# Kernel tuning notes

Hardware: AMD Instinct MI355X
Metric: run time of the kernel (lower is better)

## Reference

```python
import jax, jax.numpy as jnp
import numpy as np

N, D = 8192, 128


def setup_inputs() -> dict:
    key = jax.random.key(0)
    kx, kw, kb = jax.random.split(key, 3)
    x = jax.random.normal(kx, (N, D), dtype=jnp.float32)
    # scale projection weights so attention logits are O(1) (avoids softmax saturation)
    W = jax.random.normal(kw, (3 * D, D), dtype=jnp.float32) * 0.02
    b = jax.random.normal(kb, (3 * D,), dtype=jnp.float32) * 0.02
    return {"x": x, "W": W, "b": b}


def reference(x, W, b):
    # fused QKV projection: nn.Linear(d, 3d) -> x @ W.T + b
    qkv = x @ W.T + b              # [N, 3d]
    q, k, v = jnp.split(qkv, 3, axis=-1)  # each [N, d]
    # the original performs unscaled attention (no 1/sqrt(d)); the tiled
    # online-softmax loop computes exactly softmax(q k^T) @ v.
    s = q @ k.T                    # [N, N]
    p = jax.nn.softmax(s, axis=-1)
    return p @ v                   # [N, d]
```

## Files before the change

### kernel.cpp

```cpp
#include <hip/hip_runtime.h>
#include <hip/hip_bf16.h>

#define NROWS 8192
#define DIM 128

typedef short short8 __attribute__((ext_vector_type(8)));
typedef float f32x4 __attribute__((ext_vector_type(4)));
typedef unsigned short ushort4v __attribute__((ext_vector_type(4)));

__device__ __forceinline__ short8 asbf8(uint4 v) { return __builtin_bit_cast(short8, v); }

__device__ __forceinline__ unsigned cvtpk_bf16(float lo, float hi) {
  unsigned r;
  asm("v_cvt_pk_bf16_f32 %0, %1, %2" : "=v"(r) : "v"(lo), "v"(hi));
  return r;
}
__device__ __forceinline__ void pl32swap(unsigned& a, unsigned& b) {
  asm("v_permlane32_swap_b32 %0, %1" : "+v"(a), "+v"(b));
}
__device__ __forceinline__ void pl16swap(unsigned& a, unsigned& b) {
  asm("v_permlane16_swap_b32 %0, %1" : "+v"(a), "+v"(b));
}
__device__ __forceinline__ void gload_lds16(const void* g, void* l) {
  __builtin_amdgcn_global_load_lds(
      (const __attribute__((address_space(1))) void*)g,
      (__attribute__((address_space(3))) void*)l, 16, 0, 0);
}

__global__ __launch_bounds__(256) void qkv_proj(
    const float* __restrict__ x, const float* __restrict__ W, const float* __restrict__ bias,
    unsigned short* __restrict__ Q, unsigned short* __restrict__ K, unsigned short* __restrict__ Vt)
{
  __shared__ uint4 sX[64 * 16];
  __shared__ uint4 sW[128 * 16];

  const int mt = blockIdx.x;
  const int ct = blockIdx.y;
  const int t = threadIdx.x;

  const float4* xg = (const float4*)(x + (size_t)mt * 64 * DIM);
  const float4* wg = (const float4*)(W + (size_t)ct * 128 * DIM);
#pragma unroll
  for (int j = 0; j < 4; j++) {
    int s = t + 256 * j; int m = s >> 4, c = s & 15;
    float4 a = xg[m * 32 + 2 * c], b = xg[m * 32 + 2 * c + 1];
    sX[m * 16 + (c ^ (m & 7))] =
        (uint4){cvtpk_bf16(a.x, a.y), cvtpk_bf16(a.z, a.w), cvtpk_bf16(b.x, b.y), cvtpk_bf16(b.z, b.w)};
  }
#pragma unroll
  for (int j = 0; j < 8; j++) {
    int s = t + 256 * j; int n = s >> 4, c = s & 15;
    float4 a = wg[n * 32 + 2 * c], b = wg[n * 32 + 2 * c + 1];
    sW[n * 16 + (c ^ (n & 7))] =
        (uint4){cvtpk_bf16(a.x, a.y), cvtpk_bf16(a.z, a.w), cvtpk_bf16(b.x, b.y), cvtpk_bf16(b.z, b.w)};
  }
  __syncthreads();

  const int w = t >> 6, l = t & 63;
  const int r = l & 15, g = l >> 4, rx = r & 7;

  if (ct < 2) {
    uint4 xf[4];
#pragma unroll
    for (int f = 0; f < 4; f++) xf[f] = sX[(w * 16 + r) * 16 + ((f * 4 + g) ^ rx)];
    unsigned short* dst = (ct == 0) ? Q : K;
    const float scale = (ct == 0) ? 1.44269504088896f : 1.0f;
    const int m = mt * 64 + w * 16 + r;
#pragma unroll
    for (int ns = 0; ns < 8; ns++) {
      f32x4 acc = (f32x4){0.f, 0.f, 0.f, 0.f};
#pragma unroll
      for (int f = 0; f < 4; f++) {
        uint4 af = sW[(ns * 16 + r) * 16 + ((f * 4 + g) ^ rx)];
        acc = __builtin_amdgcn_mfma_f32_16x16x32_bf16(asbf8(af), asbf8(xf[f]), acc, 0, 0, 0);
      }
      float4 bv = *(const float4*)&bias[ct * 128 + ns * 16 + 4 * g];
      uint2 pk;
      pk.x = cvtpk_bf16((acc[0] + bv.x) * scale, (acc[1] + bv.y) * scale);
      pk.y = cvtpk_bf16((acc[2] + bv.z) * scale, (acc[3] + bv.w) * scale);
      *(uint2*)&dst[(size_t)m * DIM + ns * 16 + 4 * g] = pk;
    }
  } else {
    uint4 xf[4][4];
#pragma unroll
    for (int ms = 0; ms < 4; ms++)
#pragma unroll
      for (int f = 0; f < 4; f++) xf[ms][f] = sX[(ms * 16 + r) * 16 + ((f * 4 + g) ^ rx)];
#pragma unroll
    for (int u = 0; u < 2; u++) {
      const int n = w * 32 + u * 16 + r;
      uint4 wf[4];
#pragma unroll
      for (int f = 0; f < 4; f++) wf[f] = sW[n * 16 + ((f * 4 + g) ^ rx)];
      const float bv = bias[256 + n];
#pragma unroll
      for (int ms = 0; ms < 4; ms++) {
        f32x4 acc = (f32x4){0.f, 0.f, 0.f, 0.f};
#pragma unroll
        for (int f = 0; f < 4; f++)
          acc = __builtin_amdgcn_mfma_f32_16x16x32_bf16(asbf8(xf[ms][f]), asbf8(wf[f]), acc, 0, 0, 0);
        uint2 pk;
        pk.x = cvtpk_bf16(acc[0] + bv, acc[1] + bv);
        pk.y = cvtpk_bf16(acc[2] + bv, acc[3] + bv);
        *(uint2*)&Vt[(size_t)n * NROWS + mt * 64 + ms * 16 + 4 * g] = pk;
      }
    }
  }
}

__global__ __launch_bounds__(512, 2) void attn(
    const unsigned short* __restrict__ Q, const unsigned short* __restrict__ K,
    const unsigned short* __restrict__ Vt,
    unsigned short* __restrict__ Opb, float* __restrict__ Lp,
    float* __restrict__ outDirect, int kvlen)
{
  __shared__ uint4 sK[64 * 16];
  __shared__ uint4 sV[2][128 * 8];

  const int t = threadIdx.x;
  const int w = t >> 6, l = t & 63;
  const int r = l & 15, g = l >> 4;
  const int qt = blockIdx.x, sp = blockIdx.y;
  const int qbase = qt * 256 + w * 32;
  const int kb0 = sp * kvlen;
  const int rx = r & 7;

  const unsigned short* kgp[2];
  const unsigned short* vgp[2];
#pragma unroll
  for (int j = 0; j < 2; j++) {
    int p = t + 512 * j;
    int krow = p >> 4, kc16 = (p & 15) ^ (krow & 7);
    kgp[j] = K + (size_t)(kb0 + krow) * DIM + kc16 * 8;
    int vrow = p >> 3, vd16 = (p & 7) ^ (vrow & 7);
    vgp[j] = Vt + (size_t)vrow * NROWS + kb0 + vd16 * 8;
  }

  uint4 qf[2][4];
#pragma unroll
  for (int u = 0; u < 2; u++) {
    const uint4* Qv = (const uint4*)(Q + (size_t)(qbase + u * 16 + r) * DIM);
#pragma unroll
    for (int f = 0; f < 4; f++) qf[u][f] = Qv[f * 4 + g];
  }

  float lsum[2] = {0.f, 0.f};
  f32x4 oacc[2][8];
#pragma unroll
  for (int u = 0; u < 2; u++)
#pragma unroll
    for (int dc = 0; dc < 8; dc++) oacc[u][dc] = (f32x4){0.f, 0.f, 0.f, 0.f};

  const int niter = kvlen >> 6;

#pragma unroll
  for (int j = 0; j < 2; j++) {
    gload_lds16(kgp[j], (uint4*)sK + (t + 512 * j));
    gload_lds16(vgp[j], (uint4*)sV[0] + (t + 512 * j));
  }
  __syncthreads();

  int cur = 0;
  for (int it = 0; it < niter; ++it) {
    if (it + 1 < niter) {
      const size_t voff = (size_t)(it + 1) * 64;
#pragma unroll
      for (int j = 0; j < 2; j++)
        gload_lds16(vgp[j] + voff, (uint4*)sV[cur ^ 1] + (t + 512 * j));
    }

    f32x4 sacc[2][4];
#pragma unroll
    for (int u = 0; u < 2; u++)
#pragma unroll
      for (int kc = 0; kc < 4; kc++) sacc[u][kc] = (f32x4){0.f, 0.f, 0.f, 0.f};
#pragma unroll
    for (int kc = 0; kc < 4; kc++)
#pragma unroll
      for (int f = 0; f < 4; f++) {
        uint4 kf = sK[(kc * 16 + r) * 16 + ((f * 4 + g) ^ rx)];
        sacc[0][kc] = __builtin_amdgcn_mfma_f32_16x16x32_bf16(asbf8(kf), asbf8(qf[0][f]), sacc[0][kc], 0, 0, 0);
        sacc[1][kc] = __builtin_amdgcn_mfma_f32_16x16x32_bf16(asbf8(kf), asbf8(qf[1][f]), sacc[1][kc], 0, 0, 0);
      }

    __syncthreads();
    if (it + 1 < niter) {
      const size_t koff = (size_t)(it + 1) * 64 * DIM;
#pragma unroll
      for (int j = 0; j < 2; j++)
        gload_lds16(kgp[j] + koff, (uint4*)sK + (t + 512 * j));
    }

    unsigned c32[2][4][2];
#pragma unroll
    for (int u = 0; u < 2; u++)
#pragma unroll
      for (int kc = 0; kc < 4; kc++) {
        float p0 = __builtin_amdgcn_exp2f(sacc[u][kc][0]);
        float p1 = __builtin_amdgcn_exp2f(sacc[u][kc][1]);
        float p2 = __builtin_amdgcn_exp2f(sacc[u][kc][2]);
        float p3 = __builtin_amdgcn_exp2f(sacc[u][kc][3]);
        lsum[u] += (p0 + p1) + (p2 + p3);
        c32[u][kc][0] = cvtpk_bf16(p0, p1);
        c32[u][kc][1] = cvtpk_bf16(p2, p3);
      }

    uint4 bfrag[2][2];
#pragma unroll
    for (int u = 0; u < 2; u++)
#pragma unroll
      for (int ka = 0; ka < 2; ka++) {
        unsigned x0 = c32[u][2 * ka][0],     x1 = c32[u][2 * ka][1];
        unsigned y0 = c32[u][2 * ka + 1][0], y1 = c32[u][2 * ka + 1][1];
        pl32swap(x0, y0);
        pl16swap(x0, y0);
        pl32swap(x1, y1);
        pl16swap(x1, y1);
        bfrag[u][ka] = (uint4){x0, x1, y0, y1};
      }

#pragma unroll
    for (int dc = 0; dc < 8; dc++) {
      uint4 vf0 = sV[cur][(dc * 16 + r) * 8 + (g ^ rx)];
      uint4 vf1 = sV[cur][(dc * 16 + r) * 8 + ((4 + g) ^ rx)];
      oacc[0][dc] = __builtin_amdgcn_mfma_f32_16x16x32_bf16(asbf8(vf0), asbf8(bfrag[0][0]), oacc[0][dc], 0, 0, 0);
      oacc[0][dc] = __builtin_amdgcn_mfma_f32_16x16x32_bf16(asbf8(vf1), asbf8(bfrag[0][1]), oacc[0][dc], 0, 0, 0);
      oacc[1][dc] = __builtin_amdgcn_mfma_f32_16x16x32_bf16(asbf8(vf0), asbf8(bfrag[1][0]), oacc[1][dc], 0, 0, 0);
      oacc[1][dc] = __builtin_amdgcn_mfma_f32_16x16x32_bf16(asbf8(vf1), asbf8(bfrag[1][1]), oacc[1][dc], 0, 0, 0);
    }

    __syncthreads();
    cur ^= 1;
  }

#pragma unroll
  for (int u = 0; u < 2; u++) {
    float v = lsum[u];
    v += __shfl_xor(v, 16);
    v += __shfl_xor(v, 32);
    lsum[u] = v;
  }

  if (outDirect) {
#pragma unroll
    for (int u = 0; u < 2; u++) {
      float inv = 1.f / lsum[u];
      int q = qbase + u * 16 + r;
#pragma unroll
      for (int dc = 0; dc < 8; dc++) {
        f32x4 o = oacc[u][dc] * inv;
        *(f32x4*)&outDirect[(size_t)q * DIM + dc * 16 + 4 * g] = o;
      }
    }
  } else {
#pragma unroll
    for (int u = 0; u < 2; u++) {
      int q = qbase + u * 16 + r;
      unsigned short* po = Opb + ((size_t)sp * NROWS + q) * DIM;
#pragma unroll
      for (int dc = 0; dc < 8; dc++) {
        uint2 pk;
        pk.x = cvtpk_bf16(oacc[u][dc][0], oacc[u][dc][1]);
        pk.y = cvtpk_bf16(oacc[u][dc][2], oacc[u][dc][3]);
        *(uint2*)&po[dc * 16 + 4 * g] = pk;
      }
      if (g == 0) Lp[(size_t)sp * NROWS + q] = lsum[u];
    }
  }
}

__global__ __launch_bounds__(256) void combine(
    const unsigned short* __restrict__ Opb, const float* __restrict__ Lp,
    float* __restrict__ out, int S)
{
  int gid = blockIdx.x * 256 + threadIdx.x;
  int q = gid >> 5, d4 = gid & 31;
  float den = 0.f, n0 = 0.f, n1 = 0.f, n2 = 0.f, n3 = 0.f;
  for (int s = 0; s < S; s++) {
    den += Lp[(size_t)s * NROWS + q];
    ushort4v h = *(const ushort4v*)&Opb[((size_t)s * NROWS + q) * DIM + d4 * 4];
    n0 += __builtin_bit_cast(float, (unsigned)h[0] << 16);
    n1 += __builtin_bit_cast(float, (unsigned)h[1] << 16);
    n2 += __builtin_bit_cast(float, (unsigned)h[2] << 16);
    n3 += __builtin_bit_cast(float, (unsigned)h[3] << 16);
  }
  float inv = 1.f / den;
  float4 o = {n0 * inv, n1 * inv, n2 * inv, n3 * inv};
  *(float4*)&out[(size_t)q * DIM + d4 * 4] = o;
}

extern "C" void kernel_launch(void* const* d_in, const int* in_sizes, int n_in,
                              void* d_out, int out_size, void* d_ws, size_t ws_size,
                              hipStream_t stream)
{
  (void)in_sizes; (void)n_in; (void)out_size;
  const float* x = (const float*)d_in[0];
  const float* W = (const float*)d_in[1];
  const float* b = (const float*)d_in[2];
  float* out = (float*)d_out;
  char* ws = (char*)d_ws;

  unsigned short* Q  = (unsigned short*)ws;
  unsigned short* K  = Q + (size_t)NROWS * DIM;
  unsigned short* Vt = K + (size_t)NROWS * DIM;
  const size_t qkvB = (size_t)3 * NROWS * DIM * 2;

  auto need = [&](int S) {
    return qkvB + (size_t)S * NROWS * DIM * 2 + (size_t)S * NROWS * 4;
  };
  int S; bool direct = false;
  if      (ws_size >= need(16)) S = 16;
  else if (ws_size >= need(8))  S = 8;
  else if (ws_size >= need(4))  S = 4;
  else if (ws_size >= need(2))  S = 2;
  else if (ws_size >= need(1))  S = 1;
  else { S = 1; direct = true; }

  unsigned short* Opb = (unsigned short*)(ws + qkvB);
  float* Lp = (float*)(Opb + (size_t)S * NROWS * DIM);

  qkv_proj<<<dim3(128, 3), 256, 0, stream>>>(x, W, b, Q, K, Vt);
  attn<<<dim3(32, S), 512, 0, stream>>>(Q, K, Vt, Opb, Lp,
                                        direct ? out : nullptr, NROWS / S);
  if (!direct) combine<<<1024, 256, 0, stream>>>(Opb, Lp, out, S);
}
```

Before: 64.59 us.

## Halve attention block and KV tile, double-buffer K and V, add MFMA priority

Shrinks the attention block from 8 to 4 waves (128 query rows) and the KV tile from 64 to 32 keys, which doubles the grid along the query axis. K is now double-buffered alongside V, so both next tiles are prefetched at the top of each iteration and the mid-iteration barrier is gone. s_setprio wraps the MFMA sections to favour matrix issue. The aim is fewer barriers and more resident blocks; the cost is twice as many iterations and K/V tiles re-read from global memory by twice as many blocks.

```diff
diff --git a/kernel.cpp b/kernel.cpp
--- a/kernel.cpp
+++ b/kernel.cpp
@@ -108,20 +108,20 @@
   }
 }
 
-__global__ __launch_bounds__(512, 2) void attn(
+__global__ __launch_bounds__(256, 4) void attn(
     const unsigned short* __restrict__ Q, const unsigned short* __restrict__ K,
     const unsigned short* __restrict__ Vt,
     unsigned short* __restrict__ Opb, float* __restrict__ Lp,
     float* __restrict__ outDirect, int kvlen)
 {
-  __shared__ uint4 sK[64 * 16];
-  __shared__ uint4 sV[2][128 * 8];
+  __shared__ uint4 sK[2][32 * 16];
+  __shared__ uint4 sV[2][128 * 4];
 
   const int t = threadIdx.x;
   const int w = t >> 6, l = t & 63;
   const int r = l & 15, g = l >> 4;
   const int qt = blockIdx.x, sp = blockIdx.y;
-  const int qbase = qt * 256 + w * 32;
+  const int qbase = qt * 128 + w * 32;
   const int kb0 = sp * kvlen;
   const int rx = r & 7;
 
@@ -129,11 +129,11 @@
   const unsigned short* vgp[2];
 #pragma unroll
   for (int j = 0; j < 2; j++) {
-    int p = t + 512 * j;
+    int p = t + 256 * j;
     int krow = p >> 4, kc16 = (p & 15) ^ (krow & 7);
     kgp[j] = K + (size_t)(kb0 + krow) * DIM + kc16 * 8;
-    int vrow = p >> 3, vd16 = (p & 7) ^ (vrow & 7);
-    vgp[j] = Vt + (size_t)vrow * NROWS + kb0 + vd16 * 8;
+    int vrow = p >> 2, vs = (p & 3) ^ (vrow & 3);
+    vgp[j] = Vt + (size_t)vrow * NROWS + kb0 + vs * 8;
   }
 
   uint4 qf[2][4];
@@ -151,51 +151,49 @@
 #pragma unroll
     for (int dc = 0; dc < 8; dc++) oacc[u][dc] = (f32x4){0.f, 0.f, 0.f, 0.f};
 
-  const int niter = kvlen >> 6;
+  const int niter = kvlen >> 5;
 
 #pragma unroll
   for (int j = 0; j < 2; j++) {
-    gload_lds16(kgp[j], (uint4*)sK + (t + 512 * j));
-    gload_lds16(vgp[j], (uint4*)sV[0] + (t + 512 * j));
+    gload_lds16(kgp[j], (uint4*)sK[0] + (t + 256 * j));
+    gload_lds16(vgp[j], (uint4*)sV[0] + (t + 256 * j));
   }
   __syncthreads();
 
   int cur = 0;
   for (int it = 0; it < niter; ++it) {
     if (it + 1 < niter) {
-      const size_t voff = (size_t)(it + 1) * 64;
-#pragma unroll
-      for (int j = 0; j < 2; j++)
-        gload_lds16(vgp[j] + voff, (uint4*)sV[cur ^ 1] + (t + 512 * j));
-    }
-
-    f32x4 sacc[2][4];
+      const size_t koff = (size_t)(it + 1) * 32 * DIM;
+      const size_t voff = (size_t)(it + 1) * 32;
+      const int nb = cur ^ 1;
+#pragma unroll
+      for (int j = 0; j < 2; j++) {
+        gload_lds16(kgp[j] + koff, (uint4*)sK[nb] + (t + 256 * j));
+        gload_lds16(vgp[j] + voff, (uint4*)sV[nb] + (t + 256 * j));
+      }
+    }
+
+    f32x4 sacc[2][2];
 #pragma unroll
     for (int u = 0; u < 2; u++)
 #pragma unroll
-      for (int kc = 0; kc < 4; kc++) sacc[u][kc] = (f32x4){0.f, 0.f, 0.f, 0.f};
-#pragma unroll
-    for (int kc = 0; kc < 4; kc++)
+      for (int kc = 0; kc < 2; kc++) sacc[u][kc] = (f32x4){0.f, 0.f, 0.f, 0.f};
+    __builtin_amdgcn_s_setprio(1);
+#pragma unroll
+    for (int kc = 0; kc < 2; kc++)
 #pragma unroll
       for (int f = 0; f < 4; f++) {
-        uint4 kf = sK[(kc * 16 + r) * 16 + ((f * 4 + g) ^ rx)];
+        uint4 kf = sK[cur][(kc * 16 + r) * 16 + ((f * 4 + g) ^ rx)];
         sacc[0][kc] = __builtin_amdgcn_mfma_f32_16x16x32_bf16(asbf8(kf), asbf8(qf[0][f]), sacc[0][kc], 0, 0, 0);
         sacc[1][kc] = __builtin_amdgcn_mfma_f32_16x16x32_bf16(asbf8(kf), asbf8(qf[1][f]), sacc[1][kc], 0, 0, 0);
       }
-
-    __syncthreads();
-    if (it + 1 < niter) {
-      const size_t koff = (size_t)(it + 1) * 64 * DIM;
-#pragma unroll
-      for (int j = 0; j < 2; j++)
-        gload_lds16(kgp[j] + koff, (uint4*)sK + (t + 512 * j));
-    }
-
-    unsigned c32[2][4][2];
+    __builtin_amdgcn_s_setprio(0);
+
+    unsigned c32[2][2][2];
 #pragma unroll
     for (int u = 0; u < 2; u++)
 #pragma unroll
-      for (int kc = 0; kc < 4; kc++) {
+      for (int kc = 0; kc < 2; kc++) {
         float p0 = __builtin_amdgcn_exp2f(sacc[u][kc][0]);
         float p1 = __builtin_amdgcn_exp2f(sacc[u][kc][1]);
         float p2 = __builtin_amdgcn_exp2f(sacc[u][kc][2]);
@@ -205,29 +203,26 @@
         c32[u][kc][1] = cvtpk_bf16(p2, p3);
       }
 
-    uint4 bfrag[2][2];
-#pragma unroll
-    for (int u = 0; u < 2; u++)
-#pragma unroll
-      for (int ka = 0; ka < 2; ka++) {
-        unsigned x0 = c32[u][2 * ka][0],     x1 = c32[u][2 * ka][1];
-        unsigned y0 = c32[u][2 * ka + 1][0], y1 = c32[u][2 * ka + 1][1];
-        pl32swap(x0, y0);
-        pl16swap(x0, y0);
-        pl32swap(x1, y1);
-        pl16swap(x1, y1);
-        bfrag[u][ka] = (uint4){x0, x1, y0, y1};
-      }
-
+    uint4 bfrag[2];
+#pragma unroll
+    for (int u = 0; u < 2; u++) {
+      unsigned x0 = c32[u][0][0], x1 = c32[u][0][1];
+      unsigned y0 = c32[u][1][0], y1 = c32[u][1][1];
+      pl32swap(x0, y0);
+      pl16swap(x0, y0);
+      pl32swap(x1, y1);
+      pl16swap(x1, y1);
+      bfrag[u] = (uint4){x0, x1, y0, y1};
+    }
+
+    __builtin_amdgcn_s_setprio(1);
 #pragma unroll
     for (int dc = 0; dc < 8; dc++) {
-      uint4 vf0 = sV[cur][(dc * 16 + r) * 8 + (g ^ rx)];
-      uint4 vf1 = sV[cur][(dc * 16 + r) * 8 + ((4 + g) ^ rx)];
-      oacc[0][dc] = __builtin_amdgcn_mfma_f32_16x16x32_bf16(asbf8(vf0), asbf8(bfrag[0][0]), oacc[0][dc], 0, 0, 0);
-      oacc[0][dc] = __builtin_amdgcn_mfma_f32_16x16x32_bf16(asbf8(vf1), asbf8(bfrag[0][1]), oacc[0][dc], 0, 0, 0);
-      oacc[1][dc] = __builtin_amdgcn_mfma_f32_16x16x32_bf16(asbf8(vf0), asbf8(bfrag[1][0]), oacc[1][dc], 0, 0, 0);
-      oacc[1][dc] = __builtin_amdgcn_mfma_f32_16x16x32_bf16(asbf8(vf1), asbf8(bfrag[1][1]), oacc[1][dc], 0, 0, 0);
-    }
+      uint4 vf = sV[cur][(dc * 16 + r) * 4 + (g ^ (r & 3))];
+      oacc[0][dc] = __builtin_amdgcn_mfma_f32_16x16x32_bf16(asbf8(vf), asbf8(bfrag[0]), oacc[0][dc], 0, 0, 0);
+      oacc[1][dc] = __builtin_amdgcn_mfma_f32_16x16x32_bf16(asbf8(vf), asbf8(bfrag[1]), oacc[1][dc], 0, 0, 0);
+    }
+    __builtin_amdgcn_s_setprio(0);
 
     __syncthreads();
     cur ^= 1;
@@ -320,7 +315,7 @@
   float* Lp = (float*)(Opb + (size_t)S * NROWS * DIM);
 
   qkv_proj<<<dim3(128, 3), 256, 0, stream>>>(x, W, b, Q, K, Vt);
-  attn<<<dim3(32, S), 512, 0, stream>>>(Q, K, Vt, Opb, Lp,
+  attn<<<dim3(64, S), 256, 0, stream>>>(Q, K, Vt, Opb, Lp,
                                         direct ? out : nullptr, NROWS / S);
   if (!direct) combine<<<1024, 256, 0, stream>>>(Opb, Lp, out, S);
 }
```

Result: slower. 81.93 us (+26.8%).
